# Kernel optimization log

Measured on AMD Instinct MI355X. Metric: run time of the kernel, lower is better.

## Reference

```python
import jax, jax.numpy as jnp
import numpy as np

B, N_PER_G, H, K, A, GNN_STEPS = 64, 100, 64, 5, 50, 3
N = B * N_PER_G  # total nodes


def _lin(key, din, dout):
    s = 1.0 / np.sqrt(din)
    kw, kb = jax.random.split(key)
    w = jax.random.uniform(kw, (din, dout), minval=-s, maxval=s, dtype=jnp.float32)
    b = jax.random.uniform(kb, (dout,), minval=-s, maxval=s, dtype=jnp.float32)
    return w, b


def setup_inputs() -> dict:
    key = jax.random.key(0)
    ks = jax.random.split(key, 16)
    # complete graph (no self loops) per batch graph
    i, j = np.meshgrid(np.arange(N_PER_G), np.arange(N_PER_G), indexing="ij")
    m = i != j
    s0, d0 = i[m], j[m]  # [n*(n-1)]
    offs = (np.arange(B) * N_PER_G)[:, None]
    src = jnp.asarray((s0[None, :] + offs).reshape(-1), dtype=jnp.int32)
    dst = jnp.asarray((d0[None, :] + offs).reshape(-1), dtype=jnp.int32)
    E = src.shape[0]
    e_type = jax.random.uniform(ks[0], (E, 2), dtype=jnp.float32)
    d = jax.random.uniform(ks[1], (E, 1), dtype=jnp.float32)
    label = jax.nn.one_hot(jax.random.randint(ks[2], (N,), 0, K), K, dtype=jnp.float32)
    actions = jax.random.randint(ks[3], (B * A, 2), 0, N_PER_G)
    l1_w, l1_b = _lin(ks[4], K, H)
    l2_w, l2_b = _lin(ks[5], H, H)
    t3_w, t3_b = _lin(ks[6], H, H)
    t4_wf, t4_b = _lin(ks[7], 1, H)
    t5_wf, t5_b = _lin(ks[8], H, 1)
    t6_w, t6_b = _lin(ks[9], H, H)
    t7_1_w, t7_1_b = _lin(ks[10], H, H)
    t7_2_w, t7_2_b = _lin(ks[11], H, H)
    t9_1_w, t9_1_b = _lin(ks[12], H, H)
    t9_2_w, t9_2_b = _lin(ks[13], H, H)
    return dict(label=label, e_type=e_type, d=d,
                l1_w=l1_w, l1_b=l1_b, l2_w=l2_w, l2_b=l2_b,
                t3_w=t3_w, t3_b=t3_b, t4_w=t4_wf[0], t4_b=t4_b,
                t5_w=t5_wf[:, 0], t5_b=t5_b, t6_w=t6_w, t6_b=t6_b,
                t7_1_w=t7_1_w, t7_1_b=t7_1_b, t7_2_w=t7_2_w, t7_2_b=t7_2_b,
                t9_1_w=t9_1_w, t9_1_b=t9_1_b, t9_2_w=t9_2_w, t9_2_b=t9_2_b,
                src=src, dst=dst, actions=actions)


def reference(label, e_type, d, l1_w, l1_b, l2_w, l2_b, t3_w, t3_b, t4_w, t4_b,
              t5_w, t5_b, t6_w, t6_b, t7_1_w, t7_1_b, t7_2_w, t7_2_b,
              t9_1_w, t9_1_b, t9_2_w, t9_2_b, src, dst, actions):
    e1 = e_type[:, 0]
    # n1_hd = h[src]*e1, n1_d = d*e1; bmm(n1_hd^T, n1_d) == sum over in-edges of h[src]*e1^2*d
    w_e = (e1 * e1) * d[:, 0]                              # [E]
    s_e = d[:, 0] * e1                                     # per-edge n1_d scalar [E]
    # sum_deg relu(t4(n1_d)) as edge-parallel relu + scatter-add
    t4_edge = jax.nn.relu(s_e[:, None] * t4_w[None, :] + t4_b)   # [E,H]
    t4_sum = jax.ops.segment_sum(t4_edge, dst, num_segments=N)   # [N,H]
    base = label @ l1_w + l1_b + t4_sum @ t3_w + t3_b            # constant across gnn steps
    h = jnp.zeros((N, H), dtype=label.dtype)
    for _ in range(GNN_STEPS):
        n1_h = jax.ops.segment_sum(h[src] * w_e[:, None], dst, num_segments=N)  # [N,H]
        h = jax.nn.relu(base + n1_h @ l2_w + l2_b)
    # readout (forward_): graph mean -> t6 stem; per-action node-pair branch
    stem = h.reshape(B, N_PER_G, H).mean(axis=1) @ t6_w + t6_b    # [B,H]
    h2 = h @ t7_1_w + t7_1_b                                      # [N,H]
    offs = jnp.repeat(jnp.arange(B, dtype=actions.dtype) * N_PER_G, A)
    a = actions + offs[:, None]                                   # global node ids [B*A,2]
    ha = h2[a[:, 0]] + h2[a[:, 1]]                                # [B*A,H]
    u = jax.nn.relu(jax.nn.relu(ha) @ t7_2_w + t7_2_b) @ t9_2_w + t9_2_b
    g_branch = jax.nn.relu(stem) @ t9_1_w + t9_1_b                # [B,H]
    q = jax.nn.relu(g_branch[:, None, :] + u.reshape(B, A, H))    # [B,A,H]
    Q_sa = q.reshape(B * A, H) @ t5_w + t5_b[0]                   # [B*A]
    return Q_sa
```

## Files before the change

### kernel.cpp

```cpp
#include <hip/hip_runtime.h>

#define HD 64
#define NPG 100
#define NGRP 64
#define NACT 50
#define EPG 9900
#define HSTRIDE 409600
#define MAGICF 0x9E3779B9u

typedef const float* fcp;

__device__ __forceinline__ void publish_gather(
    float* __restrict__ buf, unsigned* __restrict__ flg,
    int g, int c, int t, float* __restrict__ hs)
{
    asm volatile("s_waitcnt vmcnt(0)" ::: "memory");
    __syncthreads();
    if (t == 0) {
        __hip_atomic_store(&flg[(g * 4 + c) * 16], MAGICF,
                           __ATOMIC_RELEASE, __HIP_MEMORY_SCOPE_AGENT);
        #pragma unroll
        for (int c2 = 0; c2 < 4; ++c2) {
            if (c2 == c) continue;
            while (__hip_atomic_load(&flg[(g * 4 + c2) * 16],
                                     __ATOMIC_RELAXED, __HIP_MEMORY_SCOPE_AGENT)
                   != MAGICF)
                __builtin_amdgcn_s_sleep(1);
        }
    }
    __syncthreads();
    __builtin_amdgcn_sched_barrier(0);
    #pragma unroll
    for (int c2 = 0; c2 < 4; ++c2) {
        if (c2 == c) continue;
        const float* src = buf + (g * NPG + c2 * 25) * HD;
        for (int idx = t; idx < 1600; idx += 512)
            hs[c2 * 1600 + idx] =
                __hip_atomic_load(src + idx, __ATOMIC_RELAXED,
                                  __HIP_MEMORY_SCOPE_AGENT);
    }
    __syncthreads();
}

__global__ __launch_bounds__(512)
void k_dqnet(fcp label, fcp e_type, fcp dvec,
             fcp l1_w, fcp l1_b, fcp l2_w, fcp l2_b,
             fcp t3_w, fcp t3_b, fcp t4_w, fcp t4_b,
             fcp t5_w, fcp t5_b, fcp t6_w, fcp t6_b,
             fcp t7_1_w, fcp t7_1_b, fcp t7_2_w, fcp t7_2_b,
             fcp t9_1_w, fcp t9_1_b, fcp t9_2_w, fcp t9_2_b,
             const int* __restrict__ actions,
             float* __restrict__ hstg, unsigned* __restrict__ flags,
             float* __restrict__ out)
{
    const int g  = blockIdx.x >> 2;
    const int c  = blockIdx.x & 3;
    const int j0 = c * 25;
    const int t  = threadIdx.x;
    const int hh = t & 63;
    const int w  = t >> 6;

    __shared__ __align__(16) float s_ld[2500];
    __shared__ __align__(16) float w_ld[2500];
    __shared__ __align__(16) float hs[NPG * HD];
    __shared__ __align__(16) float t4s[25 * HD];
    __shared__ __align__(16) float awk[8 * HD];
    __shared__ float gbuf[HD];

    float l1r[5], lab[4][5];
    #pragma unroll
    for (int kk = 0; kk < 5; ++kk) l1r[kk] = l1_w[kk * HD + hh];
    #pragma unroll
    for (int m = 0; m < 4; ++m) {
        const int jl = w + 8 * m;
        #pragma unroll
        for (int kk = 0; kk < 5; ++kk)
            lab[m][kk] = (jl < 25) ? label[(g * NPG + j0 + jl) * 5 + kk] : 0.f;
    }
    const int acnt  = (c < 2) ? 13 : 12;
    const int abase = c * 12 + (c < 2 ? c : 2);
    int a0r[2], a1r[2];
    #pragma unroll
    for (int m = 0; m < 2; ++m) {
        const int al = w + 7 * m;
        a0r[m] = 0; a1r[m] = 0;
        if (w < 7 && al < acnt) {
            const int a = g * NACT + abase + al;
            a0r[m] = actions[a * 2 + 0];
            a1r[m] = actions[a * 2 + 1];
        }
    }

    const float2* et2 = (const float2*)e_type;
    const int ebase = g * EPG;
    for (int idx = t; idx < 2500; idx += 512) {
        const int i  = idx / 25;
        const int jl = idx - i * 25;
        const int j  = j0 + jl;
        float s = 0.f, wv = 0.f;
        if (i != j) {
            const int e = ebase + i * 99 + j - (j > i ? 1 : 0);
            const float e1 = et2[e].x;
            const float dd = dvec[e];
            s  = dd * e1;
            wv = e1 * e1 * dd;
        }
        s_ld[jl * 100 + i] = s;
        w_ld[jl * 100 + i] = wv;
    }
    __syncthreads();

    const float w4  = t4_w[hh];
    const float b4  = t4_b[hh];
    const float rb4 = fmaxf(b4, 0.f);
    #pragma unroll
    for (int m = 0; m < 4; ++m) {
        const int jl = w + 8 * m;
        if (jl < 25) {
            float a0 = 0.f, a1 = 0.f, a2 = 0.f, a3 = 0.f;
            #pragma unroll 5
            for (int ib = 0; ib < 25; ++ib) {
                const float4 s4 = *(const float4*)&s_ld[jl * 100 + 4 * ib];
                a0 += fmaxf(s4.x * w4 + b4, 0.f);
                a1 += fmaxf(s4.y * w4 + b4, 0.f);
                a2 += fmaxf(s4.z * w4 + b4, 0.f);
                a3 += fmaxf(s4.w * w4 + b4, 0.f);
            }
            t4s[jl * HD + hh] = (a0 + a1) + (a2 + a3) - rb4;
        }
    }

    const float bb   = l1_b[hh] + t3_b[hh];
    const float l2bv = l2_b[hh];
    float basev[4];
    #pragma unroll
    for (int m = 0; m < 4; ++m) {
        float x = bb;
        #pragma unroll
        for (int kk = 0; kk < 5; ++kk) x += lab[m][kk] * l1r[kk];
        basev[m] = x;
    }
    for (int ib = 0; ib < 16; ++ib) {
        const float tw0 = t3_w[(4 * ib + 0) * HD + hh];
        const float tw1 = t3_w[(4 * ib + 1) * HD + hh];
        const float tw2 = t3_w[(4 * ib + 2) * HD + hh];
        const float tw3 = t3_w[(4 * ib + 3) * HD + hh];
        #pragma unroll
        for (int m = 0; m < 4; ++m) {
            const int jl = w + 8 * m;
            if (jl < 25) {
                const float4 x4 = *(const float4*)&t4s[jl * HD + 4 * ib];
                basev[m] += x4.x * tw0 + x4.y * tw1 + x4.z * tw2 + x4.w * tw3;
            }
        }
    }
    {
        float* buf = hstg;
        #pragma unroll
        for (int m = 0; m < 4; ++m) {
            const int jl = w + 8 * m;
            if (jl < 25) {
                const float hv = fmaxf(basev[m] + l2bv, 0.f);
                hs[(j0 + jl) * HD + hh] = hv;
                __hip_atomic_store(buf + (g * NPG + j0 + jl) * HD + hh, hv,
                                   __ATOMIC_RELAXED, __HIP_MEMORY_SCOPE_AGENT);
            }
        }
        publish_gather(buf, flags, g, c, t, hs);
    }

    #pragma unroll 1
    for (int step = 0; step < 2; ++step) {
        float acc[4];
        #pragma unroll
        for (int m = 0; m < 4; ++m) acc[m] = 0.f;
        for (int ib = 0; ib < 25; ++ib) {
            const float h0 = hs[(4 * ib + 0) * HD + hh];
            const float h1 = hs[(4 * ib + 1) * HD + hh];
            const float h2 = hs[(4 * ib + 2) * HD + hh];
            const float h3 = hs[(4 * ib + 3) * HD + hh];
            #pragma unroll
            for (int m = 0; m < 4; ++m) {
                const int jl = w + 8 * m;
                if (jl < 25) {
                    const float4 wv = *(const float4*)&w_ld[jl * 100 + 4 * ib];
                    acc[m] += wv.x * h0 + wv.y * h1 + wv.z * h2 + wv.w * h3;
                }
            }
        }
        #pragma unroll
        for (int m = 0; m < 4; ++m) {
            const int jl = w + 8 * m;
            if (jl < 25) t4s[jl * HD + hh] = acc[m];
        }
        float v[4];
        #pragma unroll
        for (int m = 0; m < 4; ++m) v[m] = basev[m] + l2bv;
        for (int ib = 0; ib < 16; ++ib) {
            const float w0 = l2_w[(4 * ib + 0) * HD + hh];
            const float w1 = l2_w[(4 * ib + 1) * HD + hh];
            const float w2 = l2_w[(4 * ib + 2) * HD + hh];
            const float w3 = l2_w[(4 * ib + 3) * HD + hh];
            #pragma unroll
            for (int m = 0; m < 4; ++m) {
                const int jl = w + 8 * m;
                if (jl < 25) {
                    const float4 x4 = *(const float4*)&t4s[jl * HD + 4 * ib];
                    v[m] += x4.x * w0 + x4.y * w1 + x4.z * w2 + x4.w * w3;
                }
            }
        }
        __syncthreads();
        float* buf = hstg + (1 + step) * HSTRIDE;
        unsigned* flg = flags + (1 + step) * (NGRP * 4 * 16);
        #pragma unroll
        for (int m = 0; m < 4; ++m) {
            const int jl = w + 8 * m;
            if (jl < 25) {
                const float hv = fmaxf(v[m], 0.f);
                hs[(j0 + jl) * HD + hh] = hv;
                __hip_atomic_store(buf + (g * NPG + j0 + jl) * HD + hh, hv,
                                   __ATOMIC_RELAXED, __HIP_MEMORY_SCOPE_AGENT);
            }
        }
        publish_gather(buf, flg, g, c, t, hs);
    }

    {
        float ml = 0.f;
        for (int j = w; j < NPG; j += 8) ml += hs[j * HD + hh];
        awk[w * HD + hh] = ml;
    }
    float* hsum = s_ld;
    float* r1s  = s_ld + 13 * HD;
    #pragma unroll
    for (int m = 0; m < 2; ++m) {
        const int al = w + 7 * m;
        if (w < 7 && al < acnt)
            hsum[al * HD + hh] = hs[a0r[m] * HD + hh] + hs[a1r[m] * HD + hh];
    }
    __syncthreads();

    if (w == 7) {
        float ml = 0.f;
        #pragma unroll
        for (int ww = 0; ww < 8; ++ww) ml += awk[ww * HD + hh];
        ml *= (1.f / NPG);
        float s = t6_b[hh];
        #pragma unroll 8
        for (int q = 0; q < HD; ++q) s += __shfl(ml, q, 64) * t6_w[q * HD + hh];
        s = fmaxf(s, 0.f);
        float gb = t9_1_b[hh];
        #pragma unroll 8
        for (int q = 0; q < HD; ++q) gb += __shfl(s, q, 64) * t9_1_w[q * HD + hh];
        gbuf[hh] = gb;
    } else {
        const float b71 = 2.f * t7_1_b[hh];
        float r[2];
        r[0] = b71; r[1] = b71;
        for (int ib = 0; ib < 16; ++ib) {
            const float w0 = t7_1_w[(4 * ib + 0) * HD + hh];
            const float w1 = t7_1_w[(4 * ib + 1) * HD + hh];
            const float w2 = t7_1_w[(4 * ib + 2) * HD + hh];
            const float w3 = t7_1_w[(4 * ib + 3) * HD + hh];
            #pragma unroll
            for (int m = 0; m < 2; ++m) {
                const int al = w + 7 * m;
                if (al < acnt) {
                    const float4 x4 = *(const float4*)&hsum[al * HD + 4 * ib];
                    r[m] += x4.x * w0 + x4.y * w1 + x4.z * w2 + x4.w * w3;
                }
            }
        }
        #pragma unroll
        for (int m = 0; m < 2; ++m) {
            const int al = w + 7 * m;
            if (al < acnt) r1s[al * HD + hh] = fmaxf(r[m], 0.f);
        }
        const float b72 = t7_2_b[hh];
        r[0] = b72; r[1] = b72;
        for (int ib = 0; ib < 16; ++ib) {
            const float w0 = t7_2_w[(4 * ib + 0) * HD + hh];
            const float w1 = t7_2_w[(4 * ib + 1) * HD + hh];
            const float w2 = t7_2_w[(4 * ib + 2) * HD + hh];
            const float w3 = t7_2_w[(4 * ib + 3) * HD + hh];
            #pragma unroll
            for (int m = 0; m < 2; ++m) {
                const int al = w + 7 * m;
                if (al < acnt) {
                    const float4 x4 = *(const float4*)&r1s[al * HD + 4 * ib];
                    r[m] += x4.x * w0 + x4.y * w1 + x4.z * w2 + x4.w * w3;
                }
            }
        }
        #pragma unroll
        for (int m = 0; m < 2; ++m) {
            const int al = w + 7 * m;
            if (al < acnt) hsum[al * HD + hh] = fmaxf(r[m], 0.f);
        }
    }
    __syncthreads();

    if (w < 7) {
        const float b92  = t9_2_b[hh];
        const float t5wv = t5_w[hh];
        const float t5bv = t5_b[0];
        const float gbv  = gbuf[hh];
        float u[2];
        u[0] = b92; u[1] = b92;
        for (int ib = 0; ib < 16; ++ib) {
            const float w0 = t9_2_w[(4 * ib + 0) * HD + hh];
            const float w1 = t9_2_w[(4 * ib + 1) * HD + hh];
            const float w2 = t9_2_w[(4 * ib + 2) * HD + hh];
            const float w3 = t9_2_w[(4 * ib + 3) * HD + hh];
            #pragma unroll
            for (int m = 0; m < 2; ++m) {
                const int al = w + 7 * m;
                if (al < acnt) {
                    const float4 x4 = *(const float4*)&hsum[al * HD + 4 * ib];
                    u[m] += x4.x * w0 + x4.y * w1 + x4.z * w2 + x4.w * w3;
                }
            }
        }
        #pragma unroll
        for (int m = 0; m < 2; ++m) {
            const int al = w + 7 * m;
            float qv = fmaxf(gbv + u[m], 0.f) * t5wv;
            #pragma unroll
            for (int off = 32; off > 0; off >>= 1) qv += __shfl_xor(qv, off, 64);
            if (al < acnt && hh == 0) out[g * NACT + abase + al] = qv + t5bv;
        }
    }
}

extern "C" void kernel_launch(void* const* d_in, const int* in_sizes, int n_in,
                              void* d_out, int out_size, void* d_ws, size_t ws_size,
                              hipStream_t stream)
{
    fcp label  = (fcp)d_in[0];
    fcp e_type = (fcp)d_in[1];
    fcp dvec   = (fcp)d_in[2];
    fcp l1_w   = (fcp)d_in[3];
    fcp l1_b   = (fcp)d_in[4];
    fcp l2_w   = (fcp)d_in[5];
    fcp l2_b   = (fcp)d_in[6];
    fcp t3_w   = (fcp)d_in[7];
    fcp t3_b   = (fcp)d_in[8];
    fcp t4_w   = (fcp)d_in[9];
    fcp t4_b   = (fcp)d_in[10];
    fcp t5_w   = (fcp)d_in[11];
    fcp t5_b   = (fcp)d_in[12];
    fcp t6_w   = (fcp)d_in[13];
    fcp t6_b   = (fcp)d_in[14];
    fcp t7_1_w = (fcp)d_in[15];
    fcp t7_1_b = (fcp)d_in[16];
    fcp t7_2_w = (fcp)d_in[17];
    fcp t7_2_b = (fcp)d_in[18];
    fcp t9_1_w = (fcp)d_in[19];
    fcp t9_1_b = (fcp)d_in[20];
    fcp t9_2_w = (fcp)d_in[21];
    fcp t9_2_b = (fcp)d_in[22];
    const int* actions = (const int*)d_in[25];

    char* ws = (char*)d_ws;
    float*    hstg  = (float*)ws;
    unsigned* flags = (unsigned*)(ws + 3 * 1638400);

    k_dqnet<<<dim3(NGRP * 4), dim3(512), 0, stream>>>(
        label, e_type, dvec, l1_w, l1_b, l2_w, l2_b, t3_w, t3_b, t4_w, t4_b,
        t5_w, t5_b, t6_w, t6_b, t7_1_w, t7_1_b, t7_2_w, t7_2_b,
        t9_1_w, t9_1_b, t9_2_w, t9_2_b, actions, hstg, flags, (float*)d_out);
}
```

Before: 168.5 us.

## Overlap cross-block h exchange with local aggregation using padded chunked layout

Splits the publish/wait/gather barrier so each block first aggregates over its own 25-node chunk before waiting on peer flags. It then gathers the three peer chunks with 64-bit atomic loads, interleaved with aggregation over chunks already in shared memory. The hs and edge-weight layouts are padded to 28-row chunks, with zeroed pad rows and remapped action indices, so chunk loops stay aligned. This hides inter-block sync and global-read latency behind compute, at the cost of more shared memory and extra barriers.

```diff
diff --git a/kernel.cpp b/kernel.cpp
--- a/kernel.cpp
+++ b/kernel.cpp
@@ -6,41 +6,27 @@
 #define NACT 50
 #define EPG 9900
 #define HSTRIDE 409600
+#define FLAGSTRIDE 4096
 #define MAGICF 0x9E3779B9u
 
 typedef const float* fcp;
 
-__device__ __forceinline__ void publish_gather(
-    float* __restrict__ buf, unsigned* __restrict__ flg,
-    int g, int c, int t, float* __restrict__ hs)
-{
-    asm volatile("s_waitcnt vmcnt(0)" ::: "memory");
-    __syncthreads();
-    if (t == 0) {
-        __hip_atomic_store(&flg[(g * 4 + c) * 16], MAGICF,
-                           __ATOMIC_RELEASE, __HIP_MEMORY_SCOPE_AGENT);
-        #pragma unroll
-        for (int c2 = 0; c2 < 4; ++c2) {
-            if (c2 == c) continue;
-            while (__hip_atomic_load(&flg[(g * 4 + c2) * 16],
-                                     __ATOMIC_RELAXED, __HIP_MEMORY_SCOPE_AGENT)
-                   != MAGICF)
-                __builtin_amdgcn_s_sleep(1);
-        }
-    }
-    __syncthreads();
-    __builtin_amdgcn_sched_barrier(0);
-    #pragma unroll
-    for (int c2 = 0; c2 < 4; ++c2) {
-        if (c2 == c) continue;
-        const float* src = buf + (g * NPG + c2 * 25) * HD;
-        for (int idx = t; idx < 1600; idx += 512)
-            hs[c2 * 1600 + idx] =
-                __hip_atomic_load(src + idx, __ATOMIC_RELAXED,
-                                  __HIP_MEMORY_SCOPE_AGENT);
-    }
-    __syncthreads();
-}
+#define ACC_CHUNK(CK)                                                         \
+    for (int ib = 0; ib < 7; ++ib) {                                          \
+        const float h0 = hs[((CK) * 28 + 4 * ib + 0) * HD + hh];              \
+        const float h1 = hs[((CK) * 28 + 4 * ib + 1) * HD + hh];              \
+        const float h2 = hs[((CK) * 28 + 4 * ib + 2) * HD + hh];              \
+        const float h3 = hs[((CK) * 28 + 4 * ib + 3) * HD + hh];              \
+        _Pragma("unroll")                                                     \
+        for (int m = 0; m < 4; ++m) {                                         \
+            const int jl = w + 8 * m;                                         \
+            if (jl < 25) {                                                    \
+                const float4 wv =                                             \
+                    *(const float4*)&w_pad[jl * 112 + (CK) * 28 + 4 * ib];    \
+                acc[m] += wv.x * h0 + wv.y * h1 + wv.z * h2 + wv.w * h3;      \
+            }                                                                 \
+        }                                                                     \
+    }
 
 __global__ __launch_bounds__(512)
 void k_dqnet(fcp label, fcp e_type, fcp dvec,
@@ -61,8 +47,8 @@
     const int w  = t >> 6;
 
     __shared__ __align__(16) float s_ld[2500];
-    __shared__ __align__(16) float w_ld[2500];
-    __shared__ __align__(16) float hs[NPG * HD];
+    __shared__ __align__(16) float w_pad[25 * 112];
+    __shared__ __align__(16) float hs[112 * HD];
     __shared__ __align__(16) float t4s[25 * HD];
     __shared__ __align__(16) float awk[8 * HD];
     __shared__ float gbuf[HD];
@@ -89,6 +75,17 @@
             a0r[m] = actions[a * 2 + 0];
             a1r[m] = actions[a * 2 + 1];
         }
+        a0r[m] += 3 * (a0r[m] / 25);
+        a1r[m] += 3 * (a1r[m] / 25);
+    }
+
+    for (int idx = t; idx < 768; idx += 512) {
+        const int c2 = idx / 192, r = (idx % 192) / 64, ln = idx & 63;
+        hs[(c2 * 28 + 25 + r) * HD + ln] = 0.f;
+    }
+    for (int idx = t; idx < 300; idx += 512) {
+        const int jl = idx / 12, p = idx % 12;
+        w_pad[jl * 112 + (p / 3) * 28 + 25 + (p % 3)] = 0.f;
     }
 
     const float2* et2 = (const float2*)e_type;
@@ -106,7 +103,8 @@
             wv = e1 * e1 * dd;
         }
         s_ld[jl * 100 + i] = s;
-        w_ld[jl * 100 + i] = wv;
+        const int cb = i / 25;
+        w_pad[jl * 112 + cb * 28 + (i - cb * 25)] = wv;
     }
     __syncthreads();
 
@@ -155,39 +153,74 @@
         }
     }
     {
-        float* buf = hstg;
         #pragma unroll
         for (int m = 0; m < 4; ++m) {
             const int jl = w + 8 * m;
             if (jl < 25) {
                 const float hv = fmaxf(basev[m] + l2bv, 0.f);
-                hs[(j0 + jl) * HD + hh] = hv;
-                __hip_atomic_store(buf + (g * NPG + j0 + jl) * HD + hh, hv,
+                hs[(c * 28 + jl) * HD + hh] = hv;
+                __hip_atomic_store(hstg + (g * NPG + j0 + jl) * HD + hh, hv,
                                    __ATOMIC_RELAXED, __HIP_MEMORY_SCOPE_AGENT);
             }
         }
-        publish_gather(buf, flags, g, c, t, hs);
-    }
-
+        asm volatile("s_waitcnt vmcnt(0)" ::: "memory");
+        __syncthreads();
+        if (t == 0)
+            __hip_atomic_store(&flags[(g * 4 + c) * 16], MAGICF,
+                               __ATOMIC_RELEASE, __HIP_MEMORY_SCOPE_AGENT);
+    }
+
+    const int c1 = (c + 1) & 3, c2i = (c + 2) & 3, c3 = (c + 3) & 3;
     #pragma unroll 1
     for (int step = 0; step < 2; ++step) {
+        const float* buf = hstg + step * HSTRIDE;
+        unsigned* flg = flags + step * FLAGSTRIDE;
+        float* bufn = hstg + (step + 1) * HSTRIDE;
+        unsigned* flgn = flags + (step + 1) * FLAGSTRIDE;
+
         float acc[4];
         #pragma unroll
         for (int m = 0; m < 4; ++m) acc[m] = 0.f;
-        for (int ib = 0; ib < 25; ++ib) {
-            const float h0 = hs[(4 * ib + 0) * HD + hh];
-            const float h1 = hs[(4 * ib + 1) * HD + hh];
-            const float h2 = hs[(4 * ib + 2) * HD + hh];
-            const float h3 = hs[(4 * ib + 3) * HD + hh];
-            #pragma unroll
-            for (int m = 0; m < 4; ++m) {
-                const int jl = w + 8 * m;
-                if (jl < 25) {
-                    const float4 wv = *(const float4*)&w_ld[jl * 100 + 4 * ib];
-                    acc[m] += wv.x * h0 + wv.y * h1 + wv.z * h2 + wv.w * h3;
-                }
-            }
-        }
+
+        ACC_CHUNK(c)
+
+        if (t == 0) {
+            #pragma unroll
+            for (int kk = 1; kk < 4; ++kk) {
+                const int cs = (c + kk) & 3;
+                while (__hip_atomic_load(&flg[(g * 4 + cs) * 16],
+                                         __ATOMIC_RELAXED,
+                                         __HIP_MEMORY_SCOPE_AGENT) != MAGICF)
+                    __builtin_amdgcn_s_sleep(1);
+            }
+        }
+        __syncthreads();
+
+        const double* sb = (const double*)buf;
+        const double* s1 = sb + (size_t)(g * NPG + c1 * 25) * 32;
+        const double* s2 = sb + (size_t)(g * NPG + c2i * 25) * 32;
+        const double* s3 = sb + (size_t)(g * NPG + c3 * 25) * 32;
+        double* d1 = (double*)&hs[c1 * 28 * HD];
+        double* d2 = (double*)&hs[c2i * 28 * HD];
+        double* d3 = (double*)&hs[c3 * 28 * HD];
+        const bool g2 = (t < 288);
+
+        double a0 = __hip_atomic_load(s1 + t, __ATOMIC_RELAXED, __HIP_MEMORY_SCOPE_AGENT);
+        double a1 = g2 ? __hip_atomic_load(s1 + 512 + t, __ATOMIC_RELAXED, __HIP_MEMORY_SCOPE_AGENT) : 0.0;
+        double b0 = __hip_atomic_load(s2 + t, __ATOMIC_RELAXED, __HIP_MEMORY_SCOPE_AGENT);
+        double b1 = g2 ? __hip_atomic_load(s2 + 512 + t, __ATOMIC_RELAXED, __HIP_MEMORY_SCOPE_AGENT) : 0.0;
+        d1[t] = a0; if (g2) d1[512 + t] = a1;
+        __syncthreads();
+        double e0 = __hip_atomic_load(s3 + t, __ATOMIC_RELAXED, __HIP_MEMORY_SCOPE_AGENT);
+        double e1 = g2 ? __hip_atomic_load(s3 + 512 + t, __ATOMIC_RELAXED, __HIP_MEMORY_SCOPE_AGENT) : 0.0;
+        ACC_CHUNK(c1)
+        d2[t] = b0; if (g2) d2[512 + t] = b1;
+        __syncthreads();
+        ACC_CHUNK(c2i)
+        d3[t] = e0; if (g2) d3[512 + t] = e1;
+        __syncthreads();
+        ACC_CHUNK(c3)
+
         #pragma unroll
         for (int m = 0; m < 4; ++m) {
             const int jl = w + 8 * m;
@@ -210,25 +243,52 @@
                 }
             }
         }
-        __syncthreads();
-        float* buf = hstg + (1 + step) * HSTRIDE;
-        unsigned* flg = flags + (1 + step) * (NGRP * 4 * 16);
         #pragma unroll
         for (int m = 0; m < 4; ++m) {
             const int jl = w + 8 * m;
             if (jl < 25) {
                 const float hv = fmaxf(v[m], 0.f);
-                hs[(j0 + jl) * HD + hh] = hv;
-                __hip_atomic_store(buf + (g * NPG + j0 + jl) * HD + hh, hv,
+                hs[(c * 28 + jl) * HD + hh] = hv;
+                __hip_atomic_store(bufn + (g * NPG + j0 + jl) * HD + hh, hv,
                                    __ATOMIC_RELAXED, __HIP_MEMORY_SCOPE_AGENT);
             }
         }
-        publish_gather(buf, flg, g, c, t, hs);
+        asm volatile("s_waitcnt vmcnt(0)" ::: "memory");
+        __syncthreads();
+        if (t == 0)
+            __hip_atomic_store(&flgn[(g * 4 + c) * 16], MAGICF,
+                               __ATOMIC_RELEASE, __HIP_MEMORY_SCOPE_AGENT);
+    }
+
+    {
+        const float* buf2 = hstg + 2 * HSTRIDE;
+        unsigned* flg2 = flags + 2 * FLAGSTRIDE;
+        if (t == 0) {
+            #pragma unroll
+            for (int kk = 1; kk < 4; ++kk) {
+                const int cs = (c + kk) & 3;
+                while (__hip_atomic_load(&flg2[(g * 4 + cs) * 16],
+                                         __ATOMIC_RELAXED,
+                                         __HIP_MEMORY_SCOPE_AGENT) != MAGICF)
+                    __builtin_amdgcn_s_sleep(1);
+            }
+        }
+        __syncthreads();
+        const bool g2 = (t < 288);
+        #pragma unroll
+        for (int kk = 1; kk < 4; ++kk) {
+            const int ck = (c + kk) & 3;
+            const double* s = (const double*)buf2 + (size_t)(g * NPG + ck * 25) * 32;
+            double* d = (double*)&hs[ck * 28 * HD];
+            d[t] = __hip_atomic_load(s + t, __ATOMIC_RELAXED, __HIP_MEMORY_SCOPE_AGENT);
+            if (g2) d[512 + t] = __hip_atomic_load(s + 512 + t, __ATOMIC_RELAXED, __HIP_MEMORY_SCOPE_AGENT);
+        }
+        __syncthreads();
     }
 
     {
         float ml = 0.f;
-        for (int j = w; j < NPG; j += 8) ml += hs[j * HD + hh];
+        for (int j = w; j < 112; j += 8) ml += hs[j * HD + hh];
         awk[w * HD + hh] = ml;
     }
     float* hsum = s_ld;
```

Result: faster. 162.6 us (-3.5%).
